# Kernel optimization log

Hardware: AMD Instinct MI355X
Metric: run time of the kernel (lower is better)

The kernel has to match this reference:

```python
import jax, jax.numpy as jnp
import numpy as np

# Config matching init_kwargs / input_specs
B, S = 8, 1024          # sequences, uniform seq_len (cu_seqlens = arange*S)
H, KVH, D = 32, 8, 128  # GQA: 4 query heads per kv head
BS, BPB, NB = 16, 64, 512  # block_size, blocks per seq, total blocks
T = B * S
SCALE = 0.08838834764831845  # 1/sqrt(head_dim)


def setup_inputs() -> dict:
    key = jax.random.key(0)
    kq, kk, kv = jax.random.split(key, 3)
    q = jax.random.normal(kq, (T, H * D), dtype=jnp.float32)
    k = jax.random.normal(kk, (T, KVH * D), dtype=jnp.float32)
    v = jax.random.normal(kv, (T, KVH * D), dtype=jnp.float32)
    k_cache = jnp.zeros((NB, BS, KVH, D), dtype=jnp.float32)
    v_cache = jnp.zeros((NB, BS, KVH, D), dtype=jnp.float32)
    # Contiguous page assignment: seq b uses blocks [b*BPB, (b+1)*BPB)
    block_tables = jnp.arange(B * BPB, dtype=jnp.int32).reshape(B, BPB)
    # token (b, t) -> slot block_tables[b, t//BS]*BS + t%BS == global arange here
    slot_mapping = jnp.arange(T, dtype=jnp.int32)
    return {"q": q, "k": k, "v": v, "k_cache": k_cache, "v_cache": v_cache,
            "slot_mapping": slot_mapping, "block_tables": block_tables}


def reference(q, k, v, k_cache, v_cache, slot_mapping, block_tables):
    # [T, H*D] -> [T, H, D]
    q = q.reshape(T, H, D)
    k = k.reshape(T, KVH, D)
    v = v.reshape(T, KVH, D)

    # store_kvcache: scatter new K/V into paged cache via slot_mapping
    kc = k_cache.reshape(NB * BS, KVH, D).at[slot_mapping].set(k)
    vc = v_cache.reshape(NB * BS, KVH, D).at[slot_mapping].set(v)

    # gather pages per sequence: [B, BPB, BS, KVH, D] -> [B, S, KVH, D]
    kg = kc.reshape(NB, BS, KVH, D)[block_tables].reshape(B, S, KVH, D)
    vg = vc.reshape(NB, BS, KVH, D)[block_tables].reshape(B, S, KVH, D)

    # GQA: expand kv heads to query heads
    G = H // KVH
    kg = jnp.repeat(kg, G, axis=2)  # [B, S, H, D]
    vg = jnp.repeat(vg, G, axis=2)

    qb = q.reshape(B, S, H, D)
    scores = jnp.einsum('bqhd,bkhd->bhqk', qb, kg) * SCALE  # [B, H, S, S]
    causal = jnp.tril(jnp.ones((S, S), dtype=bool))
    scores = jnp.where(causal[None, None], scores, jnp.finfo(scores.dtype).min)
    probs = jax.nn.softmax(scores, axis=-1)
    o = jnp.einsum('bhqk,bkhd->bqhd', probs, vg)  # [B, S, H, D]
    return o.reshape(T, H * D)
```

## Files before the change

kernel.cpp:

```cpp
#include <hip/hip_runtime.h>
#include <hip/hip_bf16.h>


namespace {

constexpr int Bc = 8, Sc = 1024, Hc = 32, KVHc = 8, Dc = 128;
constexpr float SCALEc = 0.08838834764831845f;
constexpr float LOG2E = 1.44269504088896f;
constexpr int KVBLK = 64;
constexpr int KD = KVHc * Dc;
constexpr int HD = Hc * Dc;
constexpr int NT = 17;
constexpr int IMG = KVBLK * Dc;

typedef __attribute__((ext_vector_type(8))) short bf16x8;
typedef __attribute__((ext_vector_type(16))) float f32x16;

__device__ __forceinline__ float exp2fast(float x) {
  return __builtin_amdgcn_exp2f(x);
}
__device__ __forceinline__ unsigned short f2bf(float f) {
  union { __hip_bfloat16 h; unsigned short u; } c;
  c.h = __float2bfloat16(f);
  return c.u;
}
__device__ __forceinline__ unsigned pack2(float a, float b) {
  return (unsigned)f2bf(a) | ((unsigned)f2bf(b) << 16);
}
__device__ __forceinline__ void pl32swap(unsigned& a, unsigned& b) {
  asm volatile("v_permlane32_swap_b32 %0, %1" : "+v"(a), "+v"(b));
}

__global__ __launch_bounds__(256) void preconv(
    const float* __restrict__ kg, const float* __restrict__ vg,
    unsigned short* __restrict__ wsK, unsigned short* __restrict__ wsV) {
  const int img = blockIdx.x;
  const int t = img & 15;
  const int kvh = (img >> 4) & 7;
  const int b = img >> 7;
  const int tid = threadIdx.x;
  const size_t row0 = (size_t)(b * Sc + t * 64);

  uint4* outK = (uint4*)(wsK + (size_t)img * IMG);
  const float* kp = kg + row0 * KD + kvh * Dc;
#pragma unroll
  for (int cc = 0; cc < 4; ++cc) {
    const int c = cc * 256 + tid;
    const int r = c >> 4, yc = c & 15;
    const int d0 = ((yc * 16) ^ ((r & 15) << 4)) >> 1;
    const float* s = kp + (size_t)r * KD + d0;
    float4 x = *(const float4*)(s);
    float4 y = *(const float4*)(s + 4);
    uint4 o;
    o.x = pack2(x.x, x.y); o.y = pack2(x.z, x.w);
    o.z = pack2(y.x, y.y); o.w = pack2(y.z, y.w);
    outK[c] = o;
  }

  __shared__ unsigned short tmp[64 * 128];
  const float* vp = vg + row0 * KD + kvh * Dc;
#pragma unroll
  for (int cc = 0; cc < 8; ++cc) {
    const int c2 = cc * 256 + tid;
    const int key = c2 >> 5, dc = (c2 & 31) * 4;
    float4 x = *(const float4*)(vp + (size_t)key * KD + dc);
    uint2 o;
    o.x = pack2(x.x, x.y); o.y = pack2(x.z, x.w);
    *(uint2*)(tmp + key * 128 + dc) = o;
  }
  __syncthreads();
  uint4* outV = (uint4*)(wsV + (size_t)img * IMG);
#pragma unroll
  for (int cc = 0; cc < 4; ++cc) {
    const int c = cc * 256 + tid;
    const int d = c >> 3, yc = c & 7;
    const int k0 = ((yc * 16) ^ ((d & 7) << 4)) >> 1;
    uint4 o;
    o.x = tmp[(k0 + 0) * 128 + d] | ((unsigned)tmp[(k0 + 1) * 128 + d] << 16);
    o.y = tmp[(k0 + 2) * 128 + d] | ((unsigned)tmp[(k0 + 3) * 128 + d] << 16);
    o.z = tmp[(k0 + 4) * 128 + d] | ((unsigned)tmp[(k0 + 5) * 128 + d] << 16);
    o.w = tmp[(k0 + 6) * 128 + d] | ((unsigned)tmp[(k0 + 7) * 128 + d] << 16);
    outV[c] = o;
  }
}

template <int ST>
__device__ __forceinline__ f32x16 qk_sub(const unsigned short* KB,
                                         const bf16x8* qf, int q32, int hi) {
  f32x16 a;
#pragma unroll
  for (int i = 0; i < 16; ++i) a[i] = 0.f;
  const int key = ST * 32 + q32;
  const char* kb = (const char*)KB + key * 256;
  const int sw = (key & 15) << 4;
#pragma unroll
  for (int ks = 0; ks < 8; ++ks) {
    bf16x8 kf = *(const bf16x8*)(kb + ((ks * 32 + hi * 16) ^ sw));
    a = __builtin_amdgcn_mfma_f32_32x32x16_bf16(kf, qf[ks], a, 0, 0, 0);
  }
  return a;
}

template <int ST>
__device__ __forceinline__ void pv_sub(const unsigned short* VB,
                                       const f32x16& p, f32x16* acc,
                                       int q32, int hi) {
  unsigned cp[8];
#pragma unroll
  for (int j = 0; j < 8; ++j) cp[j] = pack2(p[2 * j], p[2 * j + 1]);
  pl32swap(cp[0], cp[2]);
  pl32swap(cp[1], cp[3]);
  pl32swap(cp[4], cp[6]);
  pl32swap(cp[5], cp[7]);
  union { bf16x8 v; unsigned u[4]; } f0, f1;
  f0.u[0] = cp[0]; f0.u[1] = cp[1]; f0.u[2] = cp[2]; f0.u[3] = cp[3];
  f1.u[0] = cp[4]; f1.u[1] = cp[5]; f1.u[2] = cp[6]; f1.u[3] = cp[7];
#pragma unroll
  for (int ks2 = 0; ks2 < 2; ++ks2) {
    const bf16x8 pa = ks2 ? f1.v : f0.v;
#pragma unroll
    for (int dt = 0; dt < 4; ++dt) {
      const int d = dt * 32 + q32;
      const bf16x8 vf = *(const bf16x8*)(
          (const char*)VB + d * 128 +
          ((ST * 64 + ks2 * 32 + hi * 16) ^ ((d & 7) << 4)));
      acc[dt] = __builtin_amdgcn_mfma_f32_32x32x16_bf16(vf, pa, acc[dt], 0, 0, 0);
    }
  }
}

__global__ __launch_bounds__(512, 2) void attn_fwd(
    const float* __restrict__ qg,
    const unsigned short* __restrict__ wsK,
    const unsigned short* __restrict__ wsV,
    float* __restrict__ out) {
  const int bid = blockIdx.x;
  const int j   = bid >> 6;
  const int kvh = bid & 7;
  const int b   = (bid >> 3) & 7;
  const int nA  = 16 - j;
  const int bh  = b * 8 + kvh;

  const int tid = threadIdx.x;
  const int w = tid >> 6, l = tid & 63;
  const int q32 = l & 31, hi = l >> 5;
  const int h = kvh * 4 + (w >> 1);
  const int stdiag = w & 1;

  int qbase = (15 - j) * 64 + (w & 1) * 32;

  __shared__ unsigned short Kl[2][IMG];
  __shared__ unsigned short Vt[2][IMG];

  bf16x8 qf[8];
  auto LOADQ = [&](int qb_) {
    const float* qp = qg + (size_t)(b * Sc + qb_ + q32) * HD + h * Dc;
    const float sc = SCALEc * LOG2E;
#pragma unroll
    for (int ks = 0; ks < 8; ++ks) {
      const int d0 = ks * 16 + hi * 8;
      float4 x = *(const float4*)(qp + d0);
      float4 y = *(const float4*)(qp + d0 + 4);
      bf16x8 t;
      t[0] = (short)f2bf(x.x * sc); t[1] = (short)f2bf(x.y * sc);
      t[2] = (short)f2bf(x.z * sc); t[3] = (short)f2bf(x.w * sc);
      t[4] = (short)f2bf(y.x * sc); t[5] = (short)f2bf(y.y * sc);
      t[6] = (short)f2bf(y.z * sc); t[7] = (short)f2bf(y.w * sc);
      qf[ks] = t;
    }
  };
  LOADQ(qbase);

  f32x16 acc[4];
#pragma unroll
  for (int dt = 0; dt < 4; ++dt)
#pragma unroll
    for (int i = 0; i < 16; ++i) acc[dt][i] = 0.f;
  float m = -1e30f, lsum = 0.f;

  auto WRITEO = [&](int qb_) {
    const float rinv = 1.0f / lsum;
    float* ob = out + (size_t)(b * Sc + qb_ + q32) * HD + h * Dc;
#pragma unroll
    for (int dt = 0; dt < 4; ++dt)
#pragma unroll
      for (int g = 0; g < 4; ++g) {
        float4 o;
        o.x = acc[dt][g * 4 + 0] * rinv;
        o.y = acc[dt][g * 4 + 1] * rinv;
        o.z = acc[dt][g * 4 + 2] * rinv;
        o.w = acc[dt][g * 4 + 3] * rinv;
        *(float4*)(ob + dt * 32 + g * 8 + hi * 4) = o;
      }
  };

  uint4 ki0, ki1, vi0, vi1;
  auto LOAD = [&](int T) {
    const uint4* sK = (const uint4*)(wsK + ((size_t)bh * 16 + T) * IMG);
    const uint4* sV = (const uint4*)(wsV + ((size_t)bh * 16 + T) * IMG);
    ki0 = sK[tid * 2]; ki1 = sK[tid * 2 + 1];
    vi0 = sV[tid * 2]; vi1 = sV[tid * 2 + 1];
  };
  auto STORE = [&](int cb) {
    uint4* dK = (uint4*)Kl[cb];
    uint4* dV = (uint4*)Vt[cb];
    dK[tid * 2] = ki0; dK[tid * 2 + 1] = ki1;
    dV[tid * 2] = vi0; dV[tid * 2 + 1] = vi1;
  };
  auto KT = [&](int i) { return i < nA ? i : i - nA; };

  LOAD(0);
  STORE(0);
  LOAD(KT(1));
  __syncthreads();

  for (int i = 0; i < NT; ++i) {
    const int cb = i & 1;
    if (i + 1 < NT) {
      STORE(cb ^ 1);
      if (i + 2 < NT) LOAD(KT(i + 2));
    }
    if (i == nA) {
      WRITEO(qbase);
      qbase = j * 64 + (w & 1) * 32;
      LOADQ(qbase);
#pragma unroll
      for (int dt = 0; dt < 4; ++dt)
#pragma unroll
        for (int z = 0; z < 16; ++z) acc[dt][z] = 0.f;
      m = -1e30f;
      lsum = 0.f;
    }
    const int kt = KT(i);
    const unsigned short* KB = Kl[cb];
    const unsigned short* VB = Vt[cb];
    const bool last = (i == nA - 1) || (i == NT - 1);
    const bool has1 = !(last && stdiag == 0);

    f32x16 p0, p1;
    __builtin_amdgcn_s_setprio(1);
    p0 = qk_sub<0>(KB, qf, q32, hi);
    if (has1) {
      p1 = qk_sub<1>(KB, qf, q32, hi);
    } else {
#pragma unroll
      for (int z = 0; z < 16; ++z) p1[z] = -1e30f;
    }
    __builtin_amdgcn_s_setprio(0);

    if (last) {
      const int kmb = kt * KVBLK + stdiag * 32 + 4 * hi - qbase - q32;
      if (stdiag == 0) {
#pragma unroll
        for (int z = 0; z < 16; ++z) {
          const int kl = (z & 3) + 8 * (z >> 2);
          if (kmb + kl > 0) p0[z] = -1e30f;
        }
      } else {
#pragma unroll
        for (int z = 0; z < 16; ++z) {
          const int kl = (z & 3) + 8 * (z >> 2);
          if (kmb + kl > 0) p1[z] = -1e30f;
        }
      }
    }

    float t8[8];
#pragma unroll
    for (int z = 0; z < 8; ++z) t8[z] = fmaxf(p0[2 * z], p0[2 * z + 1]);
    if (has1) {
#pragma unroll
      for (int z = 0; z < 8; ++z)
        t8[z] = fmaxf(t8[z], fmaxf(p1[2 * z], p1[2 * z + 1]));
    }
    float pm = fmaxf(fmaxf(fmaxf(t8[0], t8[1]), fmaxf(t8[2], t8[3])),
                     fmaxf(fmaxf(t8[4], t8[5]), fmaxf(t8[6], t8[7])));
    pm = fmaxf(pm, __shfl_xor(pm, 32));
    if (__any(pm > m + 11.5416f)) {
      const float mn = fmaxf(m, pm);
      const float alpha = exp2fast(m - mn);
      m = mn;
      lsum *= alpha;
#pragma unroll
      for (int dt = 0; dt < 4; ++dt) acc[dt] *= alpha;
    }
    float s8[8];
#pragma unroll
    for (int z = 0; z < 16; ++z) p0[z] = exp2fast(p0[z] - m);
#pragma unroll
    for (int z = 0; z < 8; ++z) s8[z] = p0[2 * z] + p0[2 * z + 1];
    if (has1) {
#pragma unroll
      for (int z = 0; z < 16; ++z) p1[z] = exp2fast(p1[z] - m);
#pragma unroll
      for (int z = 0; z < 8; ++z) s8[z] += p1[2 * z] + p1[2 * z + 1];
    }
    float se = ((s8[0] + s8[1]) + (s8[2] + s8[3])) +
               ((s8[4] + s8[5]) + (s8[6] + s8[7]));
    se += __shfl_xor(se, 32);
    lsum += se;

    __builtin_amdgcn_s_setprio(1);
    pv_sub<0>(VB, p0, acc, q32, hi);
    if (has1) pv_sub<1>(VB, p1, acc, q32, hi);
    __builtin_amdgcn_s_setprio(0);

    __syncthreads();
  }

  WRITEO(qbase);
}

__global__ __launch_bounds__(512, 2) void attn_fwd_fb(
    const float* __restrict__ qg, const float* __restrict__ kg,
    const float* __restrict__ vg, float* __restrict__ out) {
  const int bid = blockIdx.x;
  const int j   = bid >> 6;
  const int kvh = bid & 7;
  const int b   = (bid >> 3) & 7;
  const int nA  = 16 - j;

  const int tid = threadIdx.x;
  const int w = tid >> 6, l = tid & 63;
  const int q32 = l & 31, hi = l >> 5;
  const int h = kvh * 4 + (w >> 1);
  const int stdiag = w & 1;

  int qbase = (15 - j) * 64 + (w & 1) * 32;

  __shared__ unsigned short Kl[2][KVBLK * Dc];
  __shared__ unsigned short Vt[2][Dc * KVBLK];

  bf16x8 qf[8];
  auto LOADQ = [&](int qb_) {
    const float* qp = qg + (size_t)(b * Sc + qb_ + q32) * HD + h * Dc;
#pragma unroll
    for (int ks = 0; ks < 8; ++ks) {
      const int d0 = ks * 16 + hi * 8;
      float4 x = *(const float4*)(qp + d0);
      float4 y = *(const float4*)(qp + d0 + 4);
      bf16x8 t;
      t[0] = (short)f2bf(x.x * SCALEc); t[1] = (short)f2bf(x.y * SCALEc);
      t[2] = (short)f2bf(x.z * SCALEc); t[3] = (short)f2bf(x.w * SCALEc);
      t[4] = (short)f2bf(y.x * SCALEc); t[5] = (short)f2bf(y.y * SCALEc);
      t[6] = (short)f2bf(y.z * SCALEc); t[7] = (short)f2bf(y.w * SCALEc);
      qf[ks] = t;
    }
  };
  LOADQ(qbase);

  f32x16 acc[4];
#pragma unroll
  for (int dt = 0; dt < 4; ++dt)
#pragma unroll
    for (int i = 0; i < 16; ++i) acc[dt][i] = 0.f;
  float m = -1e30f, lsum = 0.f;

  auto WRITEO = [&](int qb_) {
    const float rinv = 1.0f / lsum;
    float* ob = out + (size_t)(b * Sc + qb_ + q32) * HD + h * Dc;
#pragma unroll
    for (int dt = 0; dt < 4; ++dt)
#pragma unroll
      for (int g = 0; g < 4; ++g) {
        float4 o;
        o.x = acc[dt][g * 4 + 0] * rinv;
        o.y = acc[dt][g * 4 + 1] * rinv;
        o.z = acc[dt][g * 4 + 2] * rinv;
        o.w = acc[dt][g * 4 + 3] * rinv;
        *(float4*)(ob + dt * 32 + g * 8 + hi * 4) = o;
      }
  };

  const float* kb0 = kg + (size_t)(b * Sc) * KD + kvh * Dc;
  const float* vb0 = vg + (size_t)(b * Sc) * KD + kvh * Dc;
  const int krow = tid >> 3, kd0 = (tid & 7) * 16;
  const int vd = tid & 127, vk0 = (tid >> 7) * 16;
  float4 kreg[4];
  float vreg[16];

  auto LOAD = [&](int T) {
    const float* kp = kb0 + ((size_t)T * KVBLK + krow) * KD + kd0;
    kreg[0] = *(const float4*)(kp);
    kreg[1] = *(const float4*)(kp + 4);
    kreg[2] = *(const float4*)(kp + 8);
    kreg[3] = *(const float4*)(kp + 12);
    const float* vp = vb0 + ((size_t)T * KVBLK + vk0) * KD + vd;
#pragma unroll
    for (int jj = 0; jj < 16; ++jj) vreg[jj] = vp[(size_t)jj * KD];
  };
  auto STORE = [&](int cb) {
    unsigned short* KB = Kl[cb];
    unsigned short* VB = Vt[cb];
    uint4 A, Bq;
    A.x = pack2(kreg[0].x, kreg[0].y); A.y = pack2(kreg[0].z, kreg[0].w);
    A.z = pack2(kreg[1].x, kreg[1].y); A.w = pack2(kreg[1].z, kreg[1].w);
    Bq.x = pack2(kreg[2].x, kreg[2].y); Bq.y = pack2(kreg[2].z, kreg[2].w);
    Bq.z = pack2(kreg[3].x, kreg[3].y); Bq.w = pack2(kreg[3].z, kreg[3].w);
    const int kbase = krow * 256, ksw = (krow & 15) << 4;
    *(uint4*)((char*)KB + kbase + ((kd0 * 2) ^ ksw)) = A;
    *(uint4*)((char*)KB + kbase + ((kd0 * 2 + 16) ^ ksw)) = Bq;
    uint4 C0, C1;
    C0.x = pack2(vreg[0], vreg[1]);   C0.y = pack2(vreg[2], vreg[3]);
    C0.z = pack2(vreg[4], vreg[5]);   C0.w = pack2(vreg[6], vreg[7]);
    C1.x = pack2(vreg[8], vreg[9]);   C1.y = pack2(vreg[10], vreg[11]);
    C1.z = pack2(vreg[12], vreg[13]); C1.w = pack2(vreg[14], vreg[15]);
    const int vbase = vd * 128, vsw = (vd & 7) << 4;
    *(uint4*)((char*)VB + vbase + ((vk0 * 2) ^ vsw)) = C0;
    *(uint4*)((char*)VB + vbase + ((vk0 * 2 + 16) ^ vsw)) = C1;
  };
  auto KT = [&](int i) { return i < nA ? i : i - nA; };

  LOAD(0);
  STORE(0);
  LOAD(KT(1));
  __syncthreads();

  for (int i = 0; i < NT; ++i) {
    const int cb = i & 1;
    if (i + 1 < NT) {
      STORE(cb ^ 1);
      if (i + 2 < NT) LOAD(KT(i + 2));
    }
    if (i == nA) {
      WRITEO(qbase);
      qbase = j * 64 + (w & 1) * 32;
      LOADQ(qbase);
#pragma unroll
      for (int dt = 0; dt < 4; ++dt)
#pragma unroll
        for (int z = 0; z < 16; ++z) acc[dt][z] = 0.f;
      m = -1e30f;
      lsum = 0.f;
    }
    const int kt = KT(i);
    const unsigned short* KB = Kl[cb];
    const unsigned short* VB = Vt[cb];
    const bool last = (i == nA - 1) || (i == NT - 1);
    const bool has1 = !(last && stdiag == 0);

    f32x16 s[2];
    __builtin_amdgcn_s_setprio(1);
    s[0] = qk_sub<0>(KB, qf, q32, hi);
    if (has1) {
      s[1] = qk_sub<1>(KB, qf, q32, hi);
    } else {
#pragma unroll
      for (int z = 0; z < 16; ++z) s[1][z] = -1e30f;
    }
    __builtin_amdgcn_s_setprio(0);

    if (last) {
      const int kmb = kt * KVBLK + stdiag * 32 + 4 * hi - qbase - q32;
      if (stdiag == 0) {
#pragma unroll
        for (int z = 0; z < 16; ++z) {
          const int kl = (z & 3) + 8 * (z >> 2);
          if (kmb + kl > 0) s[0][z] = -1e30f;
        }
      } else {
#pragma unroll
        for (int z = 0; z < 16; ++z) {
          const int kl = (z & 3) + 8 * (z >> 2);
          if (kmb + kl > 0) s[1][z] = -1e30f;
        }
      }
    }

    float pm = fmaxf(s[0][0], s[1][0]);
#pragma unroll
    for (int z = 1; z < 16; ++z) pm = fmaxf(pm, fmaxf(s[0][z], s[1][z]));
    pm = fmaxf(pm, __shfl_xor(pm, 32));
    if (__any(pm > m + 8.0f)) {
      const float mn = fmaxf(m, pm);
      const float alpha = __expf(m - mn);
      m = mn;
      lsum *= alpha;
#pragma unroll
      for (int dt = 0; dt < 4; ++dt) acc[dt] *= alpha;
    }
    float se = 0.f;
#pragma unroll
    for (int z = 0; z < 16; ++z) { s[0][z] = __expf(s[0][z] - m); se += s[0][z]; }
    if (has1) {
#pragma unroll
      for (int z = 0; z < 16; ++z) { s[1][z] = __expf(s[1][z] - m); se += s[1][z]; }
    }
    se += __shfl_xor(se, 32);
    lsum += se;

    __builtin_amdgcn_s_setprio(1);
    pv_sub<0>(VB, s[0], acc, q32, hi);
    if (has1) pv_sub<1>(VB, s[1], acc, q32, hi);
    __builtin_amdgcn_s_setprio(0);

    __syncthreads();
  }

  WRITEO(qbase);
}

}

extern "C" void kernel_launch(void* const* d_in, const int* in_sizes, int n_in,
                              void* d_out, int out_size, void* d_ws, size_t ws_size,
                              hipStream_t stream) {
  const float* q = (const float*)d_in[0];
  const float* k = (const float*)d_in[1];
  const float* v = (const float*)d_in[2];
  float* out = (float*)d_out;
  const size_t need = (size_t)2 * 1024 * IMG * sizeof(unsigned short);
  if (ws_size >= need) {
    unsigned short* wsK = (unsigned short*)d_ws;
    unsigned short* wsV = wsK + (size_t)1024 * IMG;
    preconv<<<dim3(1024), dim3(256), 0, stream>>>(k, v, wsK, wsV);
    attn_fwd<<<dim3(512), dim3(512), 0, stream>>>(q, wsK, wsV, out);
  } else {
    attn_fwd_fb<<<dim3(512), dim3(512), 0, stream>>>(q, k, v, out);
  }
}
```

Baseline: 162.5 us.

## Single-buffer V tile in LDS with a separate post-PV store and barrier

Shrinks shared memory by single-buffering the V tile. K stays double-buffered, while V for the next tile is written to LDS only after the current PV step finishes, behind a second barrier. The aim is to lower LDS usage so more blocks can be resident per CU. The cost is an extra __syncthreads per iteration, and the V store can no longer overlap with the QK/softmax work.

```diff
diff --git a/kernel.cpp b/kernel.cpp
--- a/kernel.cpp
+++ b/kernel.cpp
@@ -150,7 +150,7 @@
   int qbase = (15 - j) * 64 + (w & 1) * 32;
 
   __shared__ unsigned short Kl[2][IMG];
-  __shared__ unsigned short Vt[2][IMG];
+  __shared__ unsigned short Vt[IMG];
 
   bf16x8 qf[8];
   auto LOADQ = [&](int qb_) {
@@ -195,30 +195,36 @@
   };
 
   uint4 ki0, ki1, vi0, vi1;
-  auto LOAD = [&](int T) {
+  auto LOADK = [&](int T) {
     const uint4* sK = (const uint4*)(wsK + ((size_t)bh * 16 + T) * IMG);
+    ki0 = sK[tid * 2]; ki1 = sK[tid * 2 + 1];
+  };
+  auto LOADV = [&](int T) {
     const uint4* sV = (const uint4*)(wsV + ((size_t)bh * 16 + T) * IMG);
-    ki0 = sK[tid * 2]; ki1 = sK[tid * 2 + 1];
     vi0 = sV[tid * 2]; vi1 = sV[tid * 2 + 1];
   };
-  auto STORE = [&](int cb) {
+  auto STOREK = [&](int cb) {
     uint4* dK = (uint4*)Kl[cb];
-    uint4* dV = (uint4*)Vt[cb];
     dK[tid * 2] = ki0; dK[tid * 2 + 1] = ki1;
+  };
+  auto STOREV = [&]() {
+    uint4* dV = (uint4*)Vt;
     dV[tid * 2] = vi0; dV[tid * 2 + 1] = vi1;
   };
   auto KT = [&](int i) { return i < nA ? i : i - nA; };
 
-  LOAD(0);
-  STORE(0);
-  LOAD(KT(1));
+  LOADK(0);
+  LOADV(0);
+  STOREK(0);
+  STOREV();
+  LOADK(KT(1));
+  LOADV(KT(1));
   __syncthreads();
 
   for (int i = 0; i < NT; ++i) {
-    const int cb = i & 1;
     if (i + 1 < NT) {
-      STORE(cb ^ 1);
-      if (i + 2 < NT) LOAD(KT(i + 2));
+      STOREK((i + 1) & 1);
+      if (i + 2 < NT) LOADK(KT(i + 2));
     }
     if (i == nA) {
       WRITEO(qbase);
@@ -232,8 +238,7 @@
       lsum = 0.f;
     }
     const int kt = KT(i);
-    const unsigned short* KB = Kl[cb];
-    const unsigned short* VB = Vt[cb];
+    const unsigned short* KB = Kl[i & 1];
     const bool last = (i == nA - 1) || (i == NT - 1);
     const bool has1 = !(last && stdiag == 0);
 
@@ -301,11 +306,16 @@
     lsum += se;
 
     __builtin_amdgcn_s_setprio(1);
-    pv_sub<0>(VB, p0, acc, q32, hi);
-    if (has1) pv_sub<1>(VB, p1, acc, q32, hi);
+    pv_sub<0>(Vt, p0, acc, q32, hi);
+    if (has1) pv_sub<1>(Vt, p1, acc, q32, hi);
     __builtin_amdgcn_s_setprio(0);
 
     __syncthreads();
+    if (i + 1 < NT) {
+      STOREV();
+      if (i + 2 < NT) LOADV(KT(i + 2));
+      __syncthreads();
+    }
   }
 
   WRITEO(qbase);
```

New measurement: 162.6 us. About the same (+0.1%).

## Use 1024-thread blocks covering 128-query tiles to halve K/V tile loads

Applied to the files above, without the earlier changes.

The main attention kernel now launches 256 blocks of 1024 threads. Each block handles two paired 128-row query tiles instead of two 64-row tiles, so every staged K/V tile in LDS is shared by 16 waves rather than 8. Per-wave causal bounds (lastlt) skip compute on KV tiles past each wave's diagonal, and the loop runs 18 steps. The aim is to cut global-to-LDS K/V traffic and loop iterations per query row. In exchange the block holds one CU at occupancy 1, some waves sit idle through barrier steps, and the wider block adds synchronisation cost.

```diff
diff --git a/kernel.cpp b/kernel.cpp
--- a/kernel.cpp
+++ b/kernel.cpp
@@ -10,7 +10,7 @@
 constexpr int KVBLK = 64;
 constexpr int KD = KVHc * Dc;
 constexpr int HD = Hc * Dc;
-constexpr int NT = 17;
+constexpr int NT = 18;
 constexpr int IMG = KVBLK * Dc;
 
 typedef __attribute__((ext_vector_type(8))) short bf16x8;
@@ -129,7 +129,7 @@
   }
 }
 
-__global__ __launch_bounds__(512, 2) void attn_fwd(
+__global__ __launch_bounds__(1024, 1) void attn_fwd(
     const float* __restrict__ qg,
     const unsigned short* __restrict__ wsK,
     const unsigned short* __restrict__ wsV,
@@ -138,16 +138,19 @@
   const int j   = bid >> 6;
   const int kvh = bid & 7;
   const int b   = (bid >> 3) & 7;
-  const int nA  = 16 - j;
+  const int nA  = 16 - 2 * j;
   const int bh  = b * 8 + kvh;
 
   const int tid = threadIdx.x;
   const int w = tid >> 6, l = tid & 63;
   const int q32 = l & 31, hi = l >> 5;
-  const int h = kvh * 4 + (w >> 1);
-  const int stdiag = w & 1;
-
-  int qbase = (15 - j) * 64 + (w & 1) * 32;
+  const int qsub = w & 3;
+  const int h = kvh * 4 + (w >> 2);
+  const int stdiag = qsub & 1;
+  const int lastoff = qsub >> 1;
+
+  int qbase = (7 - j) * 128 + qsub * 32;
+  int lastlt = 2 * (7 - j) + lastoff;
 
   __shared__ unsigned short Kl[2][IMG];
   __shared__ unsigned short Vt[2][IMG];
@@ -194,18 +197,14 @@
       }
   };
 
-  uint4 ki0, ki1, vi0, vi1;
+  uint4 ki, vi;
   auto LOAD = [&](int T) {
-    const uint4* sK = (const uint4*)(wsK + ((size_t)bh * 16 + T) * IMG);
-    const uint4* sV = (const uint4*)(wsV + ((size_t)bh * 16 + T) * IMG);
-    ki0 = sK[tid * 2]; ki1 = sK[tid * 2 + 1];
-    vi0 = sV[tid * 2]; vi1 = sV[tid * 2 + 1];
+    ki = ((const uint4*)(wsK + ((size_t)bh * 16 + T) * IMG))[tid];
+    vi = ((const uint4*)(wsV + ((size_t)bh * 16 + T) * IMG))[tid];
   };
   auto STORE = [&](int cb) {
-    uint4* dK = (uint4*)Kl[cb];
-    uint4* dV = (uint4*)Vt[cb];
-    dK[tid * 2] = ki0; dK[tid * 2 + 1] = ki1;
-    dV[tid * 2] = vi0; dV[tid * 2 + 1] = vi1;
+    ((uint4*)Kl[cb])[tid] = ki;
+    ((uint4*)Vt[cb])[tid] = vi;
   };
   auto KT = [&](int i) { return i < nA ? i : i - nA; };
 
@@ -222,7 +221,8 @@
     }
     if (i == nA) {
       WRITEO(qbase);
-      qbase = j * 64 + (w & 1) * 32;
+      qbase = j * 128 + qsub * 32;
+      lastlt = 2 * j + lastoff;
       LOADQ(qbase);
 #pragma unroll
       for (int dt = 0; dt < 4; ++dt)
@@ -231,79 +231,82 @@
       m = -1e30f;
       lsum = 0.f;
     }
-    const int kt = KT(i);
-    const unsigned short* KB = Kl[cb];
-    const unsigned short* VB = Vt[cb];
-    const bool last = (i == nA - 1) || (i == NT - 1);
-    const bool has1 = !(last && stdiag == 0);
-
-    f32x16 p0, p1;
-    __builtin_amdgcn_s_setprio(1);
-    p0 = qk_sub<0>(KB, qf, q32, hi);
-    if (has1) {
-      p1 = qk_sub<1>(KB, qf, q32, hi);
-    } else {
-#pragma unroll
-      for (int z = 0; z < 16; ++z) p1[z] = -1e30f;
-    }
-    __builtin_amdgcn_s_setprio(0);
-
-    if (last) {
-      const int kmb = kt * KVBLK + stdiag * 32 + 4 * hi - qbase - q32;
-      if (stdiag == 0) {
-#pragma unroll
-        for (int z = 0; z < 16; ++z) {
-          const int kl = (z & 3) + 8 * (z >> 2);
-          if (kmb + kl > 0) p0[z] = -1e30f;
+    const int lt = KT(i);
+    const bool active = (lt <= lastlt);
+    if (active) {
+      const unsigned short* KB = Kl[cb];
+      const unsigned short* VB = Vt[cb];
+      const bool last = (lt == lastlt);
+      const bool has1 = !(last && stdiag == 0);
+
+      f32x16 p0, p1;
+      __builtin_amdgcn_s_setprio(1);
+      p0 = qk_sub<0>(KB, qf, q32, hi);
+      if (has1) {
+        p1 = qk_sub<1>(KB, qf, q32, hi);
+      } else {
+#pragma unroll
+        for (int z = 0; z < 16; ++z) p1[z] = -1e30f;
+      }
+      __builtin_amdgcn_s_setprio(0);
+
+      if (last) {
+        const int kmb = lt * KVBLK + stdiag * 32 + 4 * hi - qbase - q32;
+        if (stdiag == 0) {
+#pragma unroll
+          for (int z = 0; z < 16; ++z) {
+            const int kl = (z & 3) + 8 * (z >> 2);
+            if (kmb + kl > 0) p0[z] = -1e30f;
+          }
+        } else {
+#pragma unroll
+          for (int z = 0; z < 16; ++z) {
+            const int kl = (z & 3) + 8 * (z >> 2);
+            if (kmb + kl > 0) p1[z] = -1e30f;
+          }
         }
-      } else {
-#pragma unroll
-        for (int z = 0; z < 16; ++z) {
-          const int kl = (z & 3) + 8 * (z >> 2);
-          if (kmb + kl > 0) p1[z] = -1e30f;
-        }
-      }
-    }
-
-    float t8[8];
-#pragma unroll
-    for (int z = 0; z < 8; ++z) t8[z] = fmaxf(p0[2 * z], p0[2 * z + 1]);
-    if (has1) {
-#pragma unroll
-      for (int z = 0; z < 8; ++z)
-        t8[z] = fmaxf(t8[z], fmaxf(p1[2 * z], p1[2 * z + 1]));
-    }
-    float pm = fmaxf(fmaxf(fmaxf(t8[0], t8[1]), fmaxf(t8[2], t8[3])),
-                     fmaxf(fmaxf(t8[4], t8[5]), fmaxf(t8[6], t8[7])));
-    pm = fmaxf(pm, __shfl_xor(pm, 32));
-    if (__any(pm > m + 11.5416f)) {
-      const float mn = fmaxf(m, pm);
-      const float alpha = exp2fast(m - mn);
-      m = mn;
-      lsum *= alpha;
-#pragma unroll
-      for (int dt = 0; dt < 4; ++dt) acc[dt] *= alpha;
-    }
-    float s8[8];
-#pragma unroll
-    for (int z = 0; z < 16; ++z) p0[z] = exp2fast(p0[z] - m);
-#pragma unroll
-    for (int z = 0; z < 8; ++z) s8[z] = p0[2 * z] + p0[2 * z + 1];
-    if (has1) {
-#pragma unroll
-      for (int z = 0; z < 16; ++z) p1[z] = exp2fast(p1[z] - m);
-#pragma unroll
-      for (int z = 0; z < 8; ++z) s8[z] += p1[2 * z] + p1[2 * z + 1];
-    }
-    float se = ((s8[0] + s8[1]) + (s8[2] + s8[3])) +
-               ((s8[4] + s8[5]) + (s8[6] + s8[7]));
-    se += __shfl_xor(se, 32);
-    lsum += se;
-
-    __builtin_amdgcn_s_setprio(1);
-    pv_sub<0>(VB, p0, acc, q32, hi);
-    if (has1) pv_sub<1>(VB, p1, acc, q32, hi);
-    __builtin_amdgcn_s_setprio(0);
+      }
+
+      float t8[8];
+#pragma unroll
+      for (int z = 0; z < 8; ++z) t8[z] = fmaxf(p0[2 * z], p0[2 * z + 1]);
+      if (has1) {
+#pragma unroll
+        for (int z = 0; z < 8; ++z)
+          t8[z] = fmaxf(t8[z], fmaxf(p1[2 * z], p1[2 * z + 1]));
+      }
+      float pm = fmaxf(fmaxf(fmaxf(t8[0], t8[1]), fmaxf(t8[2], t8[3])),
+                       fmaxf(fmaxf(t8[4], t8[5]), fmaxf(t8[6], t8[7])));
+      pm = fmaxf(pm, __shfl_xor(pm, 32));
+      if (__any(pm > m + 11.5416f)) {
+        const float mn = fmaxf(m, pm);
+        const float alpha = exp2fast(m - mn);
+        m = mn;
+        lsum *= alpha;
+#pragma unroll
+        for (int dt = 0; dt < 4; ++dt) acc[dt] *= alpha;
+      }
+      float s8[8];
+#pragma unroll
+      for (int z = 0; z < 16; ++z) p0[z] = exp2fast(p0[z] - m);
+#pragma unroll
+      for (int z = 0; z < 8; ++z) s8[z] = p0[2 * z] + p0[2 * z + 1];
+      if (has1) {
+#pragma unroll
+        for (int z = 0; z < 16; ++z) p1[z] = exp2fast(p1[z] - m);
+#pragma unroll
+        for (int z = 0; z < 8; ++z) s8[z] += p1[2 * z] + p1[2 * z + 1];
+      }
+      float se = ((s8[0] + s8[1]) + (s8[2] + s8[3])) +
+                 ((s8[4] + s8[5]) + (s8[6] + s8[7]));
+      se += __shfl_xor(se, 32);
+      lsum += se;
+
+      __builtin_amdgcn_s_setprio(1);
+      pv_sub<0>(VB, p0, acc, q32, hi);
+      if (has1) pv_sub<1>(VB, p1, acc, q32, hi);
+      __builtin_amdgcn_s_setprio(0);
+    }
 
     __syncthreads();
   }
@@ -416,11 +419,11 @@
   LOAD(KT(1));
   __syncthreads();
 
-  for (int i = 0; i < NT; ++i) {
+  for (int i = 0; i < 17; ++i) {
     const int cb = i & 1;
-    if (i + 1 < NT) {
+    if (i + 1 < 17) {
       STORE(cb ^ 1);
-      if (i + 2 < NT) LOAD(KT(i + 2));
+      if (i + 2 < 17) LOAD(KT(i + 2));
     }
     if (i == nA) {
       WRITEO(qbase);
@@ -436,7 +439,7 @@
     const int kt = KT(i);
     const unsigned short* KB = Kl[cb];
     const unsigned short* VB = Vt[cb];
-    const bool last = (i == nA - 1) || (i == NT - 1);
+    const bool last = (i == nA - 1) || (i == 16);
     const bool has1 = !(last && stdiag == 0);
 
     f32x16 s[2];
@@ -514,7 +517,7 @@
     unsigned short* wsK = (unsigned short*)d_ws;
     unsigned short* wsV = wsK + (size_t)1024 * IMG;
     preconv<<<dim3(1024), dim3(256), 0, stream>>>(k, v, wsK, wsV);
-    attn_fwd<<<dim3(512), dim3(512), 0, stream>>>(q, wsK, wsV, out);
+    attn_fwd<<<dim3(256), dim3(1024), 0, stream>>>(q, wsK, wsV, out);
   } else {
     attn_fwd_fb<<<dim3(512), dim3(512), 0, stream>>>(q, k, v, out);
   }
```

Result: slower. 361.4 us (+122.4%).
